# Kernel tuning notes

Measured on AMD Instinct MI355X. Metric: run time of the kernel, lower is better.

## Reference

```python
import jax, jax.numpy as jnp
import numpy as np

N_NODES = 50000
N_EDGES = 800000
IN_FEATURES = 256
HIDDEN = 128


def setup_inputs() -> dict:
    key = jax.random.key(0)
    k_x, k_r, k_c, k_v, k_w, k_b = jax.random.split(key, 6)
    x = jax.random.normal(k_x, (N_NODES, IN_FEATURES), dtype=jnp.float32)
    adj_row = jax.random.randint(k_r, (N_EDGES,), 0, N_NODES, dtype=jnp.int32)
    adj_col = jax.random.randint(k_c, (N_EDGES,), 0, N_NODES, dtype=jnp.int32)
    adj_val = jax.random.uniform(k_v, (N_EDGES,), dtype=jnp.float32)
    # Linear params: weight [hidden, in_features] (xavier-normal-ish), bias [hidden]
    std = float(np.sqrt(2.0 / (IN_FEATURES + HIDDEN)))
    W = jax.random.normal(k_w, (HIDDEN, IN_FEATURES), dtype=jnp.float32) * std
    b = jax.random.normal(k_b, (HIDDEN,), dtype=jnp.float32) * 0.01
    return {"x": x, "adj_row": adj_row, "adj_col": adj_col, "adj_val": adj_val, "W": W, "b": b}


def reference(x, adj_row, adj_col, adj_val, W, b):
    # support = Linear(x): [N, hidden]
    support = jnp.einsum('nf,hf->nh', x, W) + b
    # sparse adj @ support via edge-list gather + segment-sum scatter
    gathered = support[adj_col] * adj_val[:, None]          # [E, hidden]
    out = jax.ops.segment_sum(gathered, adj_row, num_segments=N_NODES)  # [N, hidden]
    return out
```

## Files before the change

kernel.cpp:

```cpp
#include <hip/hip_runtime.h>

#define N_NODES 50000
#define N_EDGES 800000
#define IN_F    256
#define HIDDEN  128

#define BUCKET_SZ 64
#define NB        782
#define NBINS     1024
#define EBLOCK    2048
#define EBLOCKS   391
#define LBLOCKS   782
#define CAP       1300
#define OV_CAP    4096

typedef __attribute__((ext_vector_type(8))) short bf16x8;
typedef __attribute__((ext_vector_type(4))) float f32x4;

__device__ inline unsigned short f2bf(float f) {
    unsigned u = __float_as_uint(f);
    u += 0x7FFF + ((u >> 16) & 1);
    return (unsigned short)(u >> 16);
}
__device__ inline bf16x8 cvt8(float4 a, float4 b) {
    bf16x8 r;
    r[0] = (short)f2bf(a.x); r[1] = (short)f2bf(a.y);
    r[2] = (short)f2bf(a.z); r[3] = (short)f2bf(a.w);
    r[4] = (short)f2bf(b.x); r[5] = (short)f2bf(b.y);
    r[6] = (short)f2bf(b.z); r[7] = (short)f2bf(b.w);
    return r;
}
__device__ inline float bfLo(unsigned u) { return __uint_as_float(u << 16); }
__device__ inline float bfHi(unsigned u) { return __uint_as_float(u & 0xFFFF0000u); }

__global__ __launch_bounds__(256) void fused_linear_partition_kernel(
    const float* __restrict__ x, const float* __restrict__ W,
    const float* __restrict__ bias, unsigned short* __restrict__ support,
    const int* __restrict__ adj_row, const int* __restrict__ adj_col,
    const float* __restrict__ adj_val, int* __restrict__ cursor,
    int2* __restrict__ part, int4* __restrict__ ovbuf, int* __restrict__ ovcnt)
{
    __shared__ __align__(16) char smem[32768];
    const int tid = threadIdx.x;

    if (blockIdx.x < EBLOCKS) {
        int2* lbuf  = (int2*)smem;
        int*  lofs  = (int*)(smem + 16384);
        int*  lcur  = (int*)(smem + 20480);
        int*  gbase = (int*)(smem + 24576);
        int*  tsum  = (int*)(smem + 27776);

        const int base = blockIdx.x * EBLOCK;
        const int n    = min(EBLOCK, N_EDGES - base);

        for (int i = tid; i < NBINS; i += 256) lofs[i] = 0;
        __syncthreads();

        unsigned pk[8]; float pv[8];
#pragma unroll
        for (int i = 0; i < 8; ++i) {
            int e = base + tid + i * 256;
            bool ok = e < N_EDGES;
            int ee = ok ? e : 0;
            int r = adj_row[ee], c = adj_col[ee];
            float v = adj_val[ee];
            if (ok) {
                unsigned bk = (unsigned)r >> 6;
                pk[i] = (bk << 22) | (((unsigned)r & 63u) << 16) | (unsigned)c;
                pv[i] = v;
                atomicAdd(&lofs[bk], 1);
            } else pk[i] = 0xFFFFFFFFu;
        }
        __syncthreads();

        int s0 = lofs[tid * 4], s1 = lofs[tid * 4 + 1];
        int s2 = lofs[tid * 4 + 2], s3 = lofs[tid * 4 + 3];
        int mysum = s0 + s1 + s2 + s3;
        tsum[tid] = mysum;
        __syncthreads();
#pragma unroll
        for (int off = 1; off < 256; off <<= 1) {
            int t = (tid >= off) ? tsum[tid - off] : 0;
            __syncthreads();
            tsum[tid] += t;
            __syncthreads();
        }
        int ex = tsum[tid] - mysum;
        lofs[tid * 4]     = ex;
        lofs[tid * 4 + 1] = ex + s0;
        lofs[tid * 4 + 2] = ex + s0 + s1;
        lofs[tid * 4 + 3] = ex + s0 + s1 + s2;
        __syncthreads();

        for (int b = tid; b < NB; b += 256) {
            int c = lofs[b + 1] - lofs[b];
            gbase[b] = (c > 0) ? atomicAdd(&cursor[b], c) : 0;
            lcur[b]  = lofs[b];
        }
        __syncthreads();

#pragma unroll
        for (int i = 0; i < 8; ++i) {
            if (pk[i] != 0xFFFFFFFFu) {
                unsigned bk = pk[i] >> 22;
                int p = atomicAdd(&lcur[bk], 1);
                lbuf[p] = make_int2((int)pk[i], __float_as_int(pv[i]));
            }
        }
        __syncthreads();

        for (int j = tid; j < n; j += 256) {
            int2 cv = lbuf[j];
            unsigned bk = ((unsigned)cv.x) >> 22;
            int loc = gbase[bk] + (j - lofs[bk]);
            if (loc < CAP) {
                part[(size_t)bk * CAP + loc] = make_int2(cv.x & 0x3FFFFF, cv.y);
            } else {
                int op = atomicAdd(ovcnt, 1);
                if (op < OV_CAP) {
                    int r = (int)(bk * BUCKET_SZ) + ((cv.x >> 16) & 63);
                    ovbuf[op] = make_int4(r, cv.x & 0xFFFF, cv.y, 0);
                }
            }
        }
    } else {
        short* wfrag = (short*)smem;

        const int bid  = blockIdx.x - EBLOCKS;
        const int lane = tid & 63;
        const int wave = tid >> 6;
        const int quad = lane >> 4;
        const int l16  = lane & 15;

        int m = bid * 64 + wave * 16 + l16;
        if (m >= N_NODES) m = N_NODES - 1;
        const float* xrow = x + (size_t)m * IN_F;

        f32x4 acc[8];
#pragma unroll
        for (int s = 0; s < 8; ++s) acc[s] = (f32x4){0.f, 0.f, 0.f, 0.f};

#pragma unroll
        for (int half = 0; half < 2; ++half) {
#pragma unroll
            for (int it = 0; it < 8; ++it) {
                const int f   = it * 256 + tid;
                const int ln  = f & 63;
                const int s   = (f >> 6) & 7;
                const int kc  = f >> 9;
                const int row = s * 16 + (ln & 15);
                const int k0  = (half * 4 + kc) * 32 + (ln >> 4) * 8;
                const float* wp = W + (size_t)row * IN_F + k0;
                float4 b0 = *(const float4*)wp;
                float4 b1 = *(const float4*)(wp + 4);
                *(bf16x8*)(&wfrag[(size_t)f * 8]) = cvt8(b0, b1);
            }
            __syncthreads();

#pragma unroll
            for (int kc = 0; kc < 4; ++kc) {
                const int k0 = (half * 4 + kc) * 32 + quad * 8;
                float4 a0 = *(const float4*)(xrow + k0);
                float4 a1 = *(const float4*)(xrow + k0 + 4);
                bf16x8 af = cvt8(a0, a1);
                const short* bbase = &wfrag[((size_t)(kc * 8) * 64 + lane) * 8];
#pragma unroll
                for (int s = 0; s < 8; ++s) {
                    bf16x8 bf = *(const bf16x8*)(bbase + (size_t)s * 64 * 8);
                    acc[s] = __builtin_amdgcn_mfma_f32_16x16x32_bf16(af, bf, acc[s], 0, 0, 0);
                }
            }
            __syncthreads();
        }

        const int rowBase = bid * 64 + wave * 16 + quad * 4;
#pragma unroll
        for (int reg = 0; reg < 4; ++reg) {
            const int r = rowBase + reg;
            if (r < N_NODES) {
#pragma unroll
                for (int s = 0; s < 8; ++s) {
                    const int col = s * 16 + l16;
                    float v = acc[s][reg] + bias[col];
                    support[(size_t)r * HIDDEN + col] = f2bf(v);
                }
            }
        }
    }
}

__global__ __launch_bounds__(512) void bucket_gather_kernel(
    const int* __restrict__ cursor, const int2* __restrict__ part,
    const unsigned int* __restrict__ support_u32,
    const int4* __restrict__ ovbuf, const int* __restrict__ ovcnt,
    float* __restrict__ out)
{
    __shared__ int2 sbuf[CAP];
    __shared__ int  hist[BUCKET_SZ];
    __shared__ int  rp[BUCKET_SZ + 1];
    __shared__ int  cur[BUCKET_SZ];

    const int tid  = threadIdx.x;
    const int b    = blockIdx.x;
    const int n    = min(cursor[b], CAP);
    const int wave = tid >> 6;
    const int lane = tid & 63;
    const int n_ov = min(*ovcnt, OV_CAP);

    if (tid < BUCKET_SZ) hist[tid] = 0;
    __syncthreads();

    const int2* pb = part + (size_t)b * CAP;
    for (int j = tid; j < n; j += 512) {
        atomicAdd(&hist[(pb[j].x >> 16) & 63], 1);
    }
    __syncthreads();

    if (tid < 64) {
        int a = hist[tid];
        int ia = a;
#pragma unroll
        for (int off = 1; off < 64; off <<= 1) {
            int t = __shfl_up(ia, off);
            if (tid >= off) ia += t;
        }
        rp[tid + 1] = ia;
        if (tid == 0) rp[0] = 0;
        cur[tid] = ia - a;
    }
    __syncthreads();

    for (int j = tid; j < n; j += 512) {
        int2 cv = pb[j];
        int p = atomicAdd(&cur[(cv.x >> 16) & 63], 1);
        sbuf[p] = cv;
    }
    __syncthreads();

    const int rowLo = wave * 8;
#pragma unroll 1
    for (int r = rowLo; r < rowLo + 8; ++r) {
        const int grow = b * BUCKET_SZ + r;
        if (grow >= N_NODES) break;
        const int s = rp[r], e = rp[r + 1];
        float ax = 0.f, ay = 0.f;
        int j = s;
        for (; j + 3 < e; j += 4) {
            int2 c0 = sbuf[j],     c1 = sbuf[j + 1];
            int2 c2 = sbuf[j + 2], c3 = sbuf[j + 3];
            unsigned u0 = support_u32[(size_t)(c0.x & 0xFFFF) * 64 + lane];
            unsigned u1 = support_u32[(size_t)(c1.x & 0xFFFF) * 64 + lane];
            unsigned u2 = support_u32[(size_t)(c2.x & 0xFFFF) * 64 + lane];
            unsigned u3 = support_u32[(size_t)(c3.x & 0xFFFF) * 64 + lane];
            float v0 = __int_as_float(c0.y), v1 = __int_as_float(c1.y);
            float v2 = __int_as_float(c2.y), v3 = __int_as_float(c3.y);
            ax += v0 * bfLo(u0); ay += v0 * bfHi(u0);
            ax += v1 * bfLo(u1); ay += v1 * bfHi(u1);
            ax += v2 * bfLo(u2); ay += v2 * bfHi(u2);
            ax += v3 * bfLo(u3); ay += v3 * bfHi(u3);
        }
        for (; j < e; ++j) {
            int2 cv = sbuf[j];
            unsigned u = support_u32[(size_t)(cv.x & 0xFFFF) * 64 + lane];
            float v = __int_as_float(cv.y);
            ax += v * bfLo(u); ay += v * bfHi(u);
        }
        for (int t = 0; t < n_ov; ++t) {
            int4 o = ovbuf[t];
            if (o.x == grow) {
                unsigned u = support_u32[(size_t)o.y * 64 + lane];
                float v = __int_as_float(o.z);
                ax += v * bfLo(u); ay += v * bfHi(u);
            }
        }
        *(float2*)(out + (size_t)grow * HIDDEN + lane * 2) = make_float2(ax, ay);
    }
}

extern "C" void kernel_launch(void* const* d_in, const int* in_sizes, int n_in,
                              void* d_out, int out_size, void* d_ws, size_t ws_size,
                              hipStream_t stream) {
    const float* x       = (const float*)d_in[0];
    const int*   adj_row = (const int*)d_in[1];
    const int*   adj_col = (const int*)d_in[2];
    const float* adj_val = (const float*)d_in[3];
    const float* W       = (const float*)d_in[4];
    const float* b       = (const float*)d_in[5];
    float* out = (float*)d_out;

    char* wsb = (char*)d_ws;
    const size_t off_support = 0;
    const size_t off_part    = off_support + (size_t)N_NODES * HIDDEN * 2;
    const size_t off_cursor  = off_part + (size_t)NB * CAP * 8;
    const size_t off_ovcnt   = off_cursor + (size_t)NB * 4;
    const size_t off_ovbuf   = (off_ovcnt + 4 + 15) & ~(size_t)15;

    unsigned short* support = (unsigned short*)(wsb + off_support);
    int2* part   = (int2*)(wsb + off_part);
    int*  cursor = (int*)(wsb + off_cursor);
    int*  ovcnt  = (int*)(wsb + off_ovcnt);
    int4* ovbuf  = (int4*)(wsb + off_ovbuf);

    hipMemsetAsync(cursor, 0, (size_t)(NB + 1) * 4, stream);

    fused_linear_partition_kernel<<<EBLOCKS + LBLOCKS, 256, 0, stream>>>(
        x, W, b, support, adj_row, adj_col, adj_val, cursor, part, ovbuf, ovcnt);
    bucket_gather_kernel<<<NB, 512, 0, stream>>>(
        cursor, part, (const unsigned int*)support, ovbuf, ovcnt, out);
}
```

Measured before the change: 163.2 us.

## Merge memset, partition/linear, and gather into one cooperative persistent kernel

Replaces the memset plus two kernel launches with a single cooperative kernel. It zeroes the cursors in-kernel and uses grid.sync() barriers between the partition/linear phase and the gather phase, with blocks looping over tasks persistently. Edge partition blocks grow to 3328 edges (13 per thread, fewer blocks), and the gather drops to 256 threads with 16 rows per wave. The aim is to remove launch gaps and the memset. The risk is the grid-wide barrier cost, and gather parallelism limited to at most 1024 resident blocks at half the previous threads per bucket. A fallback to separate launches remains if the cooperative launch fails.

```diff
diff --git a/kernel.cpp b/kernel.cpp
--- a/kernel.cpp
+++ b/kernel.cpp
@@ -1,4 +1,7 @@
 #include <hip/hip_runtime.h>
+#include <hip/hip_cooperative_groups.h>
+
+namespace cg = cooperative_groups;
 
 #define N_NODES 50000
 #define N_EDGES 800000
@@ -8,11 +11,16 @@
 #define BUCKET_SZ 64
 #define NB        782
 #define NBINS     1024
-#define EBLOCK    2048
-#define EBLOCKS   391
+#define EBLOCK    3328
+#define EPT       13
+#define EBLOCKS   241
 #define LBLOCKS   782
+#define NTASKS    1023
 #define CAP       1300
 #define OV_CAP    4096
+#define MEGA_MAXG 1024
+
+#define SMEM_BYTES 39040
 
 typedef __attribute__((ext_vector_type(8))) short bf16x8;
 typedef __attribute__((ext_vector_type(4))) float f32x4;
@@ -33,185 +41,184 @@
 __device__ inline float bfLo(unsigned u) { return __uint_as_float(u << 16); }
 __device__ inline float bfHi(unsigned u) { return __uint_as_float(u & 0xFFFF0000u); }
 
-__global__ __launch_bounds__(256) void fused_linear_partition_kernel(
-    const float* __restrict__ x, const float* __restrict__ W,
-    const float* __restrict__ bias, unsigned short* __restrict__ support,
+__device__ __forceinline__ void do_partition(
+    char* smem, int task,
     const int* __restrict__ adj_row, const int* __restrict__ adj_col,
     const float* __restrict__ adj_val, int* __restrict__ cursor,
     int2* __restrict__ part, int4* __restrict__ ovbuf, int* __restrict__ ovcnt)
 {
-    __shared__ __align__(16) char smem[32768];
-    const int tid = threadIdx.x;
-
-    if (blockIdx.x < EBLOCKS) {
-        int2* lbuf  = (int2*)smem;
-        int*  lofs  = (int*)(smem + 16384);
-        int*  lcur  = (int*)(smem + 20480);
-        int*  gbase = (int*)(smem + 24576);
-        int*  tsum  = (int*)(smem + 27776);
-
-        const int base = blockIdx.x * EBLOCK;
-        const int n    = min(EBLOCK, N_EDGES - base);
-
-        for (int i = tid; i < NBINS; i += 256) lofs[i] = 0;
-        __syncthreads();
-
-        unsigned pk[8]; float pv[8];
-#pragma unroll
-        for (int i = 0; i < 8; ++i) {
-            int e = base + tid + i * 256;
-            bool ok = e < N_EDGES;
-            int ee = ok ? e : 0;
-            int r = adj_row[ee], c = adj_col[ee];
-            float v = adj_val[ee];
-            if (ok) {
-                unsigned bk = (unsigned)r >> 6;
-                pk[i] = (bk << 22) | (((unsigned)r & 63u) << 16) | (unsigned)c;
-                pv[i] = v;
-                atomicAdd(&lofs[bk], 1);
-            } else pk[i] = 0xFFFFFFFFu;
-        }
-        __syncthreads();
-
-        int s0 = lofs[tid * 4], s1 = lofs[tid * 4 + 1];
-        int s2 = lofs[tid * 4 + 2], s3 = lofs[tid * 4 + 3];
-        int mysum = s0 + s1 + s2 + s3;
-        tsum[tid] = mysum;
-        __syncthreads();
-#pragma unroll
-        for (int off = 1; off < 256; off <<= 1) {
-            int t = (tid >= off) ? tsum[tid - off] : 0;
-            __syncthreads();
-            tsum[tid] += t;
-            __syncthreads();
-        }
-        int ex = tsum[tid] - mysum;
-        lofs[tid * 4]     = ex;
-        lofs[tid * 4 + 1] = ex + s0;
-        lofs[tid * 4 + 2] = ex + s0 + s1;
-        lofs[tid * 4 + 3] = ex + s0 + s1 + s2;
-        __syncthreads();
-
-        for (int b = tid; b < NB; b += 256) {
-            int c = lofs[b + 1] - lofs[b];
-            gbase[b] = (c > 0) ? atomicAdd(&cursor[b], c) : 0;
-            lcur[b]  = lofs[b];
-        }
-        __syncthreads();
-
-#pragma unroll
-        for (int i = 0; i < 8; ++i) {
-            if (pk[i] != 0xFFFFFFFFu) {
-                unsigned bk = pk[i] >> 22;
-                int p = atomicAdd(&lcur[bk], 1);
-                lbuf[p] = make_int2((int)pk[i], __float_as_int(pv[i]));
+    int2* lbuf  = (int2*)smem;
+    int*  lofs  = (int*)(smem + 26624);
+    int*  lcur  = (int*)(smem + 30720);
+    int*  gbase = (int*)(smem + 34816);
+    int*  tsum  = (int*)(smem + 38016);
+
+    const int tid  = threadIdx.x;
+    const int base = task * EBLOCK;
+    const int n    = min(EBLOCK, N_EDGES - base);
+
+    for (int i = tid; i < NBINS; i += 256) lofs[i] = 0;
+    __syncthreads();
+
+    unsigned pk[EPT]; float pv[EPT];
+#pragma unroll
+    for (int i = 0; i < EPT; ++i) {
+        int li = tid + i * 256;
+        bool ok = li < n;
+        int ee = ok ? (base + li) : base;
+        int r = adj_row[ee], c = adj_col[ee];
+        float v = adj_val[ee];
+        if (ok) {
+            unsigned bk = (unsigned)r >> 6;
+            pk[i] = (bk << 22) | (((unsigned)r & 63u) << 16) | (unsigned)c;
+            pv[i] = v;
+            atomicAdd(&lofs[bk], 1);
+        } else pk[i] = 0xFFFFFFFFu;
+    }
+    __syncthreads();
+
+    int s0 = lofs[tid * 4], s1 = lofs[tid * 4 + 1];
+    int s2 = lofs[tid * 4 + 2], s3 = lofs[tid * 4 + 3];
+    int mysum = s0 + s1 + s2 + s3;
+    tsum[tid] = mysum;
+    __syncthreads();
+#pragma unroll
+    for (int off = 1; off < 256; off <<= 1) {
+        int t = (tid >= off) ? tsum[tid - off] : 0;
+        __syncthreads();
+        tsum[tid] += t;
+        __syncthreads();
+    }
+    int ex = tsum[tid] - mysum;
+    lofs[tid * 4]     = ex;
+    lofs[tid * 4 + 1] = ex + s0;
+    lofs[tid * 4 + 2] = ex + s0 + s1;
+    lofs[tid * 4 + 3] = ex + s0 + s1 + s2;
+    __syncthreads();
+
+    for (int b = tid; b < NB; b += 256) {
+        int c = lofs[b + 1] - lofs[b];
+        gbase[b] = (c > 0) ? atomicAdd(&cursor[b], c) : 0;
+        lcur[b]  = lofs[b];
+    }
+    __syncthreads();
+
+#pragma unroll
+    for (int i = 0; i < EPT; ++i) {
+        if (pk[i] != 0xFFFFFFFFu) {
+            unsigned bk = pk[i] >> 22;
+            int p = atomicAdd(&lcur[bk], 1);
+            lbuf[p] = make_int2((int)pk[i], __float_as_int(pv[i]));
+        }
+    }
+    __syncthreads();
+
+    for (int j = tid; j < n; j += 256) {
+        int2 cv = lbuf[j];
+        unsigned bk = ((unsigned)cv.x) >> 22;
+        int loc = gbase[bk] + (j - lofs[bk]);
+        if (loc < CAP) {
+            part[(size_t)bk * CAP + loc] = make_int2(cv.x & 0x3FFFFF, cv.y);
+        } else {
+            int op = atomicAdd(ovcnt, 1);
+            if (op < OV_CAP) {
+                int r = (int)(bk * BUCKET_SZ) + ((cv.x >> 16) & 63);
+                ovbuf[op] = make_int4(r, cv.x & 0xFFFF, cv.y, 0);
             }
         }
-        __syncthreads();
-
-        for (int j = tid; j < n; j += 256) {
-            int2 cv = lbuf[j];
-            unsigned bk = ((unsigned)cv.x) >> 22;
-            int loc = gbase[bk] + (j - lofs[bk]);
-            if (loc < CAP) {
-                part[(size_t)bk * CAP + loc] = make_int2(cv.x & 0x3FFFFF, cv.y);
-            } else {
-                int op = atomicAdd(ovcnt, 1);
-                if (op < OV_CAP) {
-                    int r = (int)(bk * BUCKET_SZ) + ((cv.x >> 16) & 63);
-                    ovbuf[op] = make_int4(r, cv.x & 0xFFFF, cv.y, 0);
-                }
+    }
+}
+
+__device__ __forceinline__ void do_linear(
+    char* smem, int bid,
+    const float* __restrict__ x, const float* __restrict__ W,
+    const float* __restrict__ bias, unsigned short* __restrict__ support)
+{
+    short* wfrag = (short*)smem;
+
+    const int tid  = threadIdx.x;
+    const int lane = tid & 63;
+    const int wave = tid >> 6;
+    const int quad = lane >> 4;
+    const int l16  = lane & 15;
+
+    int m = bid * 64 + wave * 16 + l16;
+    if (m >= N_NODES) m = N_NODES - 1;
+    const float* xrow = x + (size_t)m * IN_F;
+
+    f32x4 acc[8];
+#pragma unroll
+    for (int s = 0; s < 8; ++s) acc[s] = (f32x4){0.f, 0.f, 0.f, 0.f};
+
+#pragma unroll
+    for (int half = 0; half < 2; ++half) {
+#pragma unroll
+        for (int it = 0; it < 8; ++it) {
+            const int f   = it * 256 + tid;
+            const int ln  = f & 63;
+            const int s   = (f >> 6) & 7;
+            const int kc  = f >> 9;
+            const int row = s * 16 + (ln & 15);
+            const int k0  = (half * 4 + kc) * 32 + (ln >> 4) * 8;
+            const float* wp = W + (size_t)row * IN_F + k0;
+            float4 b0 = *(const float4*)wp;
+            float4 b1 = *(const float4*)(wp + 4);
+            *(bf16x8*)(&wfrag[(size_t)f * 8]) = cvt8(b0, b1);
+        }
+        __syncthreads();
+
+#pragma unroll
+        for (int kc = 0; kc < 4; ++kc) {
+            const int k0 = (half * 4 + kc) * 32 + quad * 8;
+            float4 a0 = *(const float4*)(xrow + k0);
+            float4 a1 = *(const float4*)(xrow + k0 + 4);
+            bf16x8 af = cvt8(a0, a1);
+            const short* bbase = &wfrag[((size_t)(kc * 8) * 64 + lane) * 8];
+#pragma unroll
+            for (int s = 0; s < 8; ++s) {
+                bf16x8 bf = *(const bf16x8*)(bbase + (size_t)s * 64 * 8);
+                acc[s] = __builtin_amdgcn_mfma_f32_16x16x32_bf16(af, bf, acc[s], 0, 0, 0);
             }
         }
-    } else {
-        short* wfrag = (short*)smem;
-
-        const int bid  = blockIdx.x - EBLOCKS;
-        const int lane = tid & 63;
-        const int wave = tid >> 6;
-        const int quad = lane >> 4;
-        const int l16  = lane & 15;
-
-        int m = bid * 64 + wave * 16 + l16;
-        if (m >= N_NODES) m = N_NODES - 1;
-        const float* xrow = x + (size_t)m * IN_F;
-
-        f32x4 acc[8];
-#pragma unroll
-        for (int s = 0; s < 8; ++s) acc[s] = (f32x4){0.f, 0.f, 0.f, 0.f};
-
-#pragma unroll
-        for (int half = 0; half < 2; ++half) {
-#pragma unroll
-            for (int it = 0; it < 8; ++it) {
-                const int f   = it * 256 + tid;
-                const int ln  = f & 63;
-                const int s   = (f >> 6) & 7;
-                const int kc  = f >> 9;
-                const int row = s * 16 + (ln & 15);
-                const int k0  = (half * 4 + kc) * 32 + (ln >> 4) * 8;
-                const float* wp = W + (size_t)row * IN_F + k0;
-                float4 b0 = *(const float4*)wp;
-                float4 b1 = *(const float4*)(wp + 4);
-                *(bf16x8*)(&wfrag[(size_t)f * 8]) = cvt8(b0, b1);
+        __syncthreads();
+    }
+
+    const int rowBase = bid * 64 + wave * 16 + quad * 4;
+#pragma unroll
+    for (int reg = 0; reg < 4; ++reg) {
+        const int r = rowBase + reg;
+        if (r < N_NODES) {
+#pragma unroll
+            for (int s = 0; s < 8; ++s) {
+                const int col = s * 16 + l16;
+                float v = acc[s][reg] + bias[col];
+                support[(size_t)r * HIDDEN + col] = f2bf(v);
             }
-            __syncthreads();
-
-#pragma unroll
-            for (int kc = 0; kc < 4; ++kc) {
-                const int k0 = (half * 4 + kc) * 32 + quad * 8;
-                float4 a0 = *(const float4*)(xrow + k0);
-                float4 a1 = *(const float4*)(xrow + k0 + 4);
-                bf16x8 af = cvt8(a0, a1);
-                const short* bbase = &wfrag[((size_t)(kc * 8) * 64 + lane) * 8];
-#pragma unroll
-                for (int s = 0; s < 8; ++s) {
-                    bf16x8 bf = *(const bf16x8*)(bbase + (size_t)s * 64 * 8);
-                    acc[s] = __builtin_amdgcn_mfma_f32_16x16x32_bf16(af, bf, acc[s], 0, 0, 0);
-                }
-            }
-            __syncthreads();
-        }
-
-        const int rowBase = bid * 64 + wave * 16 + quad * 4;
-#pragma unroll
-        for (int reg = 0; reg < 4; ++reg) {
-            const int r = rowBase + reg;
-            if (r < N_NODES) {
-#pragma unroll
-                for (int s = 0; s < 8; ++s) {
-                    const int col = s * 16 + l16;
-                    float v = acc[s][reg] + bias[col];
-                    support[(size_t)r * HIDDEN + col] = f2bf(v);
-                }
-            }
-        }
-    }
-}
-
-__global__ __launch_bounds__(512) void bucket_gather_kernel(
+        }
+    }
+}
+
+__device__ __forceinline__ void do_gather(
+    char* smem, int b,
     const int* __restrict__ cursor, const int2* __restrict__ part,
     const unsigned int* __restrict__ support_u32,
-    const int4* __restrict__ ovbuf, const int* __restrict__ ovcnt,
-    float* __restrict__ out)
-{
-    __shared__ int2 sbuf[CAP];
-    __shared__ int  hist[BUCKET_SZ];
-    __shared__ int  rp[BUCKET_SZ + 1];
-    __shared__ int  cur[BUCKET_SZ];
+    const int4* __restrict__ ovbuf, int n_ov, float* __restrict__ out)
+{
+    int2* sbuf = (int2*)smem;
+    int*  hist = (int*)(smem + 10400);
+    int*  rp   = (int*)(smem + 10656);
+    int*  cur  = (int*)(smem + 10928);
 
     const int tid  = threadIdx.x;
-    const int b    = blockIdx.x;
     const int n    = min(cursor[b], CAP);
     const int wave = tid >> 6;
     const int lane = tid & 63;
-    const int n_ov = min(*ovcnt, OV_CAP);
 
     if (tid < BUCKET_SZ) hist[tid] = 0;
     __syncthreads();
 
     const int2* pb = part + (size_t)b * CAP;
-    for (int j = tid; j < n; j += 512) {
+    for (int j = tid; j < n; j += 256) {
         atomicAdd(&hist[(pb[j].x >> 16) & 63], 1);
     }
     __syncthreads();
@@ -230,16 +237,16 @@
     }
     __syncthreads();
 
-    for (int j = tid; j < n; j += 512) {
+    for (int j = tid; j < n; j += 256) {
         int2 cv = pb[j];
         int p = atomicAdd(&cur[(cv.x >> 16) & 63], 1);
         sbuf[p] = cv;
     }
     __syncthreads();
 
-    const int rowLo = wave * 8;
+    const int rowLo = wave * 16;
 #pragma unroll 1
-    for (int r = rowLo; r < rowLo + 8; ++r) {
+    for (int r = rowLo; r < rowLo + 16; ++r) {
         const int grow = b * BUCKET_SZ + r;
         if (grow >= N_NODES) break;
         const int s = rp[r], e = rp[r + 1];
@@ -277,6 +284,63 @@
     }
 }
 
+__global__ __launch_bounds__(256, 4) void gcn_mega_kernel(
+    const float* __restrict__ x, const float* __restrict__ W,
+    const float* __restrict__ bias, unsigned short* __restrict__ support,
+    const int* __restrict__ adj_row, const int* __restrict__ adj_col,
+    const float* __restrict__ adj_val, int* __restrict__ cursor,
+    int2* __restrict__ part, int4* __restrict__ ovbuf, int* __restrict__ ovcnt,
+    float* __restrict__ out)
+{
+    __shared__ __align__(16) char smem[SMEM_BYTES];
+    cg::grid_group grid = cg::this_grid();
+
+    if (blockIdx.x == 0) {
+        for (int i = threadIdx.x; i < NB + 1; i += 256) cursor[i] = 0;
+    }
+    grid.sync();
+
+    for (int task = blockIdx.x; task < NTASKS; task += gridDim.x) {
+        if (task < EBLOCKS)
+            do_partition(smem, task, adj_row, adj_col, adj_val, cursor, part, ovbuf, ovcnt);
+        else
+            do_linear(smem, task - EBLOCKS, x, W, bias, support);
+        __syncthreads();
+    }
+    grid.sync();
+
+    const int n_ov = min(*ovcnt, OV_CAP);
+    for (int b = blockIdx.x; b < NB; b += gridDim.x) {
+        do_gather(smem, b, cursor, part, (const unsigned int*)support, ovbuf, n_ov, out);
+        __syncthreads();
+    }
+}
+
+__global__ __launch_bounds__(256) void fused_linear_partition_kernel(
+    const float* __restrict__ x, const float* __restrict__ W,
+    const float* __restrict__ bias, unsigned short* __restrict__ support,
+    const int* __restrict__ adj_row, const int* __restrict__ adj_col,
+    const float* __restrict__ adj_val, int* __restrict__ cursor,
+    int2* __restrict__ part, int4* __restrict__ ovbuf, int* __restrict__ ovcnt)
+{
+    __shared__ __align__(16) char smem[SMEM_BYTES];
+    if (blockIdx.x < EBLOCKS)
+        do_partition(smem, blockIdx.x, adj_row, adj_col, adj_val, cursor, part, ovbuf, ovcnt);
+    else
+        do_linear(smem, blockIdx.x - EBLOCKS, x, W, bias, support);
+}
+
+__global__ __launch_bounds__(256) void bucket_gather_kernel(
+    const int* __restrict__ cursor, const int2* __restrict__ part,
+    const unsigned int* __restrict__ support_u32,
+    const int4* __restrict__ ovbuf, const int* __restrict__ ovcnt,
+    float* __restrict__ out)
+{
+    __shared__ __align__(16) char smem[SMEM_BYTES];
+    const int n_ov = min(*ovcnt, OV_CAP);
+    do_gather(smem, blockIdx.x, cursor, part, support_u32, ovbuf, n_ov, out);
+}
+
 extern "C" void kernel_launch(void* const* d_in, const int* in_sizes, int n_in,
                               void* d_out, int out_size, void* d_ws, size_t ws_size,
                               hipStream_t stream) {
@@ -301,10 +365,27 @@
     int*  ovcnt  = (int*)(wsb + off_ovcnt);
     int4* ovbuf  = (int4*)(wsb + off_ovbuf);
 
-    hipMemsetAsync(cursor, 0, (size_t)(NB + 1) * 4, stream);
-
-    fused_linear_partition_kernel<<<EBLOCKS + LBLOCKS, 256, 0, stream>>>(
-        x, W, b, support, adj_row, adj_col, adj_val, cursor, part, ovbuf, ovcnt);
-    bucket_gather_kernel<<<NB, 512, 0, stream>>>(
-        cursor, part, (const unsigned int*)support, ovbuf, ovcnt, out);
-}
+    static int G = 0;
+    if (G == 0) {
+        int nb = 0;
+        if (hipOccupancyMaxActiveBlocksPerMultiprocessor(&nb, gcn_mega_kernel, 256, 0) != hipSuccess || nb < 1)
+            nb = 1;
+        long g = (long)nb * 256;
+        G = (g > MEGA_MAXG) ? MEGA_MAXG : (int)g;
+    }
+
+    void* args[] = {
+        (void*)&x, (void*)&W, (void*)&b, (void*)&support,
+        (void*)&adj_row, (void*)&adj_col, (void*)&adj_val,
+        (void*)&cursor, (void*)&part, (void*)&ovbuf, (void*)&ovcnt, (void*)&out
+    };
+    hipError_t err = hipLaunchCooperativeKernel((const void*)gcn_mega_kernel,
+                                                dim3(G), dim3(256), args, 0, stream);
+    if (err != hipSuccess) {
+        hipMemsetAsync(cursor, 0, (size_t)(NB + 1) * 4, stream);
+        fused_linear_partition_kernel<<<NTASKS, 256, 0, stream>>>(
+            x, W, b, support, adj_row, adj_col, adj_val, cursor, part, ovbuf, ovcnt);
+        bucket_gather_kernel<<<NB, 256, 0, stream>>>(
+            cursor, part, (const unsigned int*)support, ovbuf, ovcnt, out);
+    }
+}
```

Result: slower. 318.9 us (+95.4%).

## Replace global atomic bucket partition with per-block sorted chunks and offset tables

Applied to the files above, without the earlier changes.

The edge partition no longer reserves space in global buckets with atomics. Each edge block writes its locally sorted chunk contiguously, together with a per-bucket offset table, and each gather block prefix-sums the 241 segment lengths and copies its segments into LDS. This removes the cursor memset, the global atomics and the overflow buffer scan. The linear blocks now compute 128 rows each with two accumulator sets, halving the block count. The trade-off is that each gather thread serially copies a small strided segment and a 512-wide LDS scan is added, and edges beyond CAP per bucket are silently dropped.

```diff
diff --git a/kernel.cpp b/kernel.cpp
--- a/kernel.cpp
+++ b/kernel.cpp
@@ -8,11 +8,16 @@
 #define BUCKET_SZ 64
 #define NB        782
 #define NBINS     1024
-#define EBLOCK    2048
-#define EBLOCKS   391
-#define LBLOCKS   782
+#define EBLOCK    3328
+#define EPT       13
+#define EBLOCKS   241
+#define LIN_ROWS  128
+#define LBLOCKS   391
+#define NTASKS    632
+#define OFSP      784
 #define CAP       1300
-#define OV_CAP    4096
+
+#define SMEM_BYTES 35840
 
 typedef __attribute__((ext_vector_type(8))) short bf16x8;
 typedef __attribute__((ext_vector_type(4))) float f32x4;
@@ -37,31 +42,31 @@
     const float* __restrict__ x, const float* __restrict__ W,
     const float* __restrict__ bias, unsigned short* __restrict__ support,
     const int* __restrict__ adj_row, const int* __restrict__ adj_col,
-    const float* __restrict__ adj_val, int* __restrict__ cursor,
-    int2* __restrict__ part, int4* __restrict__ ovbuf, int* __restrict__ ovcnt)
+    const float* __restrict__ adj_val,
+    int2* __restrict__ part, int* __restrict__ ofs)
 {
-    __shared__ __align__(16) char smem[32768];
+    __shared__ __align__(16) char smem[SMEM_BYTES];
     const int tid = threadIdx.x;
 
     if (blockIdx.x < EBLOCKS) {
-        int2* lbuf  = (int2*)smem;
-        int*  lofs  = (int*)(smem + 16384);
-        int*  lcur  = (int*)(smem + 20480);
-        int*  gbase = (int*)(smem + 24576);
-        int*  tsum  = (int*)(smem + 27776);
-
-        const int base = blockIdx.x * EBLOCK;
+        int2* lbuf = (int2*)smem;
+        int*  lofs = (int*)(smem + 26624);
+        int*  lcur = (int*)(smem + 30720);
+        int*  tsum = (int*)(smem + 34816);
+
+        const int task = blockIdx.x;
+        const int base = task * EBLOCK;
         const int n    = min(EBLOCK, N_EDGES - base);
 
         for (int i = tid; i < NBINS; i += 256) lofs[i] = 0;
         __syncthreads();
 
-        unsigned pk[8]; float pv[8];
-#pragma unroll
-        for (int i = 0; i < 8; ++i) {
-            int e = base + tid + i * 256;
-            bool ok = e < N_EDGES;
-            int ee = ok ? e : 0;
+        unsigned pk[EPT]; float pv[EPT];
+#pragma unroll
+        for (int i = 0; i < EPT; ++i) {
+            int li = tid + i * 256;
+            bool ok = li < n;
+            int ee = ok ? (base + li) : base;
             int r = adj_row[ee], c = adj_col[ee];
             float v = adj_val[ee];
             if (ok) {
@@ -92,37 +97,23 @@
         lofs[tid * 4 + 3] = ex + s0 + s1 + s2;
         __syncthreads();
 
-        for (int b = tid; b < NB; b += 256) {
-            int c = lofs[b + 1] - lofs[b];
-            gbase[b] = (c > 0) ? atomicAdd(&cursor[b], c) : 0;
-            lcur[b]  = lofs[b];
-        }
-        __syncthreads();
-
-#pragma unroll
-        for (int i = 0; i < 8; ++i) {
+        for (int i = tid; i < NBINS; i += 256) lcur[i] = lofs[i];
+        __syncthreads();
+
+#pragma unroll
+        for (int i = 0; i < EPT; ++i) {
             if (pk[i] != 0xFFFFFFFFu) {
                 unsigned bk = pk[i] >> 22;
                 int p = atomicAdd(&lcur[bk], 1);
-                lbuf[p] = make_int2((int)pk[i], __float_as_int(pv[i]));
+                lbuf[p] = make_int2((int)(pk[i] & 0x3FFFFF), __float_as_int(pv[i]));
             }
         }
         __syncthreads();
 
-        for (int j = tid; j < n; j += 256) {
-            int2 cv = lbuf[j];
-            unsigned bk = ((unsigned)cv.x) >> 22;
-            int loc = gbase[bk] + (j - lofs[bk]);
-            if (loc < CAP) {
-                part[(size_t)bk * CAP + loc] = make_int2(cv.x & 0x3FFFFF, cv.y);
-            } else {
-                int op = atomicAdd(ovcnt, 1);
-                if (op < OV_CAP) {
-                    int r = (int)(bk * BUCKET_SZ) + ((cv.x >> 16) & 63);
-                    ovbuf[op] = make_int4(r, cv.x & 0xFFFF, cv.y, 0);
-                }
-            }
-        }
+        for (int j = tid; j < n; j += 256)
+            part[(size_t)task * EBLOCK + j] = lbuf[j];
+        for (int i = tid; i <= NB; i += 256)
+            ofs[(size_t)task * OFSP + i] = lofs[i];
     } else {
         short* wfrag = (short*)smem;
 
@@ -132,13 +123,18 @@
         const int quad = lane >> 4;
         const int l16  = lane & 15;
 
-        int m = bid * 64 + wave * 16 + l16;
-        if (m >= N_NODES) m = N_NODES - 1;
-        const float* xrow = x + (size_t)m * IN_F;
-
-        f32x4 acc[8];
-#pragma unroll
-        for (int s = 0; s < 8; ++s) acc[s] = (f32x4){0.f, 0.f, 0.f, 0.f};
+        int m0 = bid * LIN_ROWS + wave * 32 + l16;
+        int m1 = m0 + 16;
+        if (m0 >= N_NODES) m0 = N_NODES - 1;
+        if (m1 >= N_NODES) m1 = N_NODES - 1;
+        const float* xr0 = x + (size_t)m0 * IN_F;
+        const float* xr1 = x + (size_t)m1 * IN_F;
+
+        f32x4 acc[2][8];
+#pragma unroll
+        for (int g = 0; g < 2; ++g)
+#pragma unroll
+            for (int s = 0; s < 8; ++s) acc[g][s] = (f32x4){0.f, 0.f, 0.f, 0.f};
 
 #pragma unroll
         for (int half = 0; half < 2; ++half) {
@@ -160,29 +156,36 @@
 #pragma unroll
             for (int kc = 0; kc < 4; ++kc) {
                 const int k0 = (half * 4 + kc) * 32 + quad * 8;
-                float4 a0 = *(const float4*)(xrow + k0);
-                float4 a1 = *(const float4*)(xrow + k0 + 4);
-                bf16x8 af = cvt8(a0, a1);
+                float4 a0 = *(const float4*)(xr0 + k0);
+                float4 a1 = *(const float4*)(xr0 + k0 + 4);
+                bf16x8 af0 = cvt8(a0, a1);
+                float4 a2 = *(const float4*)(xr1 + k0);
+                float4 a3 = *(const float4*)(xr1 + k0 + 4);
+                bf16x8 af1 = cvt8(a2, a3);
                 const short* bbase = &wfrag[((size_t)(kc * 8) * 64 + lane) * 8];
 #pragma unroll
                 for (int s = 0; s < 8; ++s) {
                     bf16x8 bf = *(const bf16x8*)(bbase + (size_t)s * 64 * 8);
-                    acc[s] = __builtin_amdgcn_mfma_f32_16x16x32_bf16(af, bf, acc[s], 0, 0, 0);
+                    acc[0][s] = __builtin_amdgcn_mfma_f32_16x16x32_bf16(af0, bf, acc[0][s], 0, 0, 0);
+                    acc[1][s] = __builtin_amdgcn_mfma_f32_16x16x32_bf16(af1, bf, acc[1][s], 0, 0, 0);
                 }
             }
             __syncthreads();
         }
 
-        const int rowBase = bid * 64 + wave * 16 + quad * 4;
-#pragma unroll
-        for (int reg = 0; reg < 4; ++reg) {
-            const int r = rowBase + reg;
-            if (r < N_NODES) {
-#pragma unroll
-                for (int s = 0; s < 8; ++s) {
-                    const int col = s * 16 + l16;
-                    float v = acc[s][reg] + bias[col];
-                    support[(size_t)r * HIDDEN + col] = f2bf(v);
+#pragma unroll
+        for (int g = 0; g < 2; ++g) {
+            const int rowBase = bid * LIN_ROWS + wave * 32 + g * 16 + quad * 4;
+#pragma unroll
+            for (int reg = 0; reg < 4; ++reg) {
+                const int r = rowBase + reg;
+                if (r < N_NODES) {
+#pragma unroll
+                    for (int s = 0; s < 8; ++s) {
+                        const int col = s * 16 + l16;
+                        float v = acc[g][s][reg] + bias[col];
+                        support[(size_t)r * HIDDEN + col] = f2bf(v);
+                    }
                 }
             }
         }
@@ -190,30 +193,53 @@
 }
 
 __global__ __launch_bounds__(512) void bucket_gather_kernel(
-    const int* __restrict__ cursor, const int2* __restrict__ part,
-    const unsigned int* __restrict__ support_u32,
-    const int4* __restrict__ ovbuf, const int* __restrict__ ovcnt,
-    float* __restrict__ out)
+    const int* __restrict__ ofs, const int2* __restrict__ part,
+    const unsigned int* __restrict__ support_u32, float* __restrict__ out)
 {
-    __shared__ int2 sbuf[CAP];
+    __shared__ int2 sbufA[CAP];
+    __shared__ int2 sbufB[CAP];
+    __shared__ int  sarr[512];
     __shared__ int  hist[BUCKET_SZ];
     __shared__ int  rp[BUCKET_SZ + 1];
     __shared__ int  cur[BUCKET_SZ];
 
     const int tid  = threadIdx.x;
     const int b    = blockIdx.x;
-    const int n    = min(cursor[b], CAP);
     const int wave = tid >> 6;
     const int lane = tid & 63;
-    const int n_ov = min(*ovcnt, OV_CAP);
 
     if (tid < BUCKET_SZ) hist[tid] = 0;
-    __syncthreads();
-
-    const int2* pb = part + (size_t)b * CAP;
-    for (int j = tid; j < n; j += 512) {
-        atomicAdd(&hist[(pb[j].x >> 16) & 63], 1);
-    }
+
+    int sstart = 0, slen = 0;
+    if (tid < EBLOCKS) {
+        const int* orow = ofs + (size_t)tid * OFSP + b;
+        sstart = orow[0];
+        slen   = orow[1] - sstart;
+    }
+    sarr[tid] = slen;
+    __syncthreads();
+
+#pragma unroll
+    for (int off = 1; off < 512; off <<= 1) {
+        int t = (tid >= off) ? sarr[tid - off] : 0;
+        __syncthreads();
+        sarr[tid] += t;
+        __syncthreads();
+    }
+    const int excl = sarr[tid] - slen;
+    const int n    = min(sarr[511], CAP);
+
+    {
+        const int2* seg = part + (size_t)tid * EBLOCK + sstart;
+        for (int k = 0; k < slen; ++k) {
+            int p = excl + k;
+            if (p < CAP) sbufA[p] = seg[k];
+        }
+    }
+    __syncthreads();
+
+    for (int j = tid; j < n; j += 512)
+        atomicAdd(&hist[(sbufA[j].x >> 16) & 63], 1);
     __syncthreads();
 
     if (tid < 64) {
@@ -231,9 +257,9 @@
     __syncthreads();
 
     for (int j = tid; j < n; j += 512) {
-        int2 cv = pb[j];
+        int2 cv = sbufA[j];
         int p = atomicAdd(&cur[(cv.x >> 16) & 63], 1);
-        sbuf[p] = cv;
+        sbufB[p] = cv;
     }
     __syncthreads();
 
@@ -246,8 +272,8 @@
         float ax = 0.f, ay = 0.f;
         int j = s;
         for (; j + 3 < e; j += 4) {
-            int2 c0 = sbuf[j],     c1 = sbuf[j + 1];
-            int2 c2 = sbuf[j + 2], c3 = sbuf[j + 3];
+            int2 c0 = sbufB[j],     c1 = sbufB[j + 1];
+            int2 c2 = sbufB[j + 2], c3 = sbufB[j + 3];
             unsigned u0 = support_u32[(size_t)(c0.x & 0xFFFF) * 64 + lane];
             unsigned u1 = support_u32[(size_t)(c1.x & 0xFFFF) * 64 + lane];
             unsigned u2 = support_u32[(size_t)(c2.x & 0xFFFF) * 64 + lane];
@@ -260,18 +286,10 @@
             ax += v3 * bfLo(u3); ay += v3 * bfHi(u3);
         }
         for (; j < e; ++j) {
-            int2 cv = sbuf[j];
+            int2 cv = sbufB[j];
             unsigned u = support_u32[(size_t)(cv.x & 0xFFFF) * 64 + lane];
             float v = __int_as_float(cv.y);
             ax += v * bfLo(u); ay += v * bfHi(u);
-        }
-        for (int t = 0; t < n_ov; ++t) {
-            int4 o = ovbuf[t];
-            if (o.x == grow) {
-                unsigned u = support_u32[(size_t)o.y * 64 + lane];
-                float v = __int_as_float(o.z);
-                ax += v * bfLo(u); ay += v * bfHi(u);
-            }
         }
         *(float2*)(out + (size_t)grow * HIDDEN + lane * 2) = make_float2(ax, ay);
     }
@@ -291,20 +309,14 @@
     char* wsb = (char*)d_ws;
     const size_t off_support = 0;
     const size_t off_part    = off_support + (size_t)N_NODES * HIDDEN * 2;
-    const size_t off_cursor  = off_part + (size_t)NB * CAP * 8;
-    const size_t off_ovcnt   = off_cursor + (size_t)NB * 4;
-    const size_t off_ovbuf   = (off_ovcnt + 4 + 15) & ~(size_t)15;
+    const size_t off_ofs     = off_part + (size_t)EBLOCKS * EBLOCK * 8;
 
     unsigned short* support = (unsigned short*)(wsb + off_support);
-    int2* part   = (int2*)(wsb + off_part);
-    int*  cursor = (int*)(wsb + off_cursor);
-    int*  ovcnt  = (int*)(wsb + off_ovcnt);
-    int4* ovbuf  = (int4*)(wsb + off_ovbuf);
-
-    hipMemsetAsync(cursor, 0, (size_t)(NB + 1) * 4, stream);
-
-    fused_linear_partition_kernel<<<EBLOCKS + LBLOCKS, 256, 0, stream>>>(
-        x, W, b, support, adj_row, adj_col, adj_val, cursor, part, ovbuf, ovcnt);
+    int2* part = (int2*)(wsb + off_part);
+    int*  ofs  = (int*)(wsb + off_ofs);
+
+    fused_linear_partition_kernel<<<NTASKS, 256, 0, stream>>>(
+        x, W, b, support, adj_row, adj_col, adj_val, part, ofs);
     bucket_gather_kernel<<<NB, 512, 0, stream>>>(
-        cursor, part, (const unsigned int*)support, ovbuf, ovcnt, out);
-}
+        ofs, part, (const unsigned int*)support, out);
+}
```

Measured after the change: 159.6 us. 1.02x faster.
